# Optimization experiments

Hardware: AMD Instinct MI355X
Metric: run time of the kernel (lower is better)

The kernel has to match this reference:

```python
import jax, jax.numpy as jnp
import numpy as np

B, T, C = 2, 4096, 768
H = 12
D = C // H  # head_dim = 64

def setup_inputs() -> dict:
    key = jax.random.key(0)
    ks = jax.random.split(key, 5)
    s = 1.0 / np.sqrt(C)
    return {
        "x": jax.random.normal(ks[0], (B, T, C), dtype=jnp.float32),
        "qkv_w": jax.random.normal(ks[1], (C, 3 * C), dtype=jnp.float32) * s,
        "qkv_b": jax.random.normal(ks[2], (3 * C,), dtype=jnp.float32) * 0.02,
        "out_w": jax.random.normal(ks[3], (C, C), dtype=jnp.float32) * s,
        "out_b": jax.random.normal(ks[4], (C,), dtype=jnp.float32) * 0.02,
    }

def reference(x, qkv_w, qkv_b, out_w, out_b):
    b, t, c = x.shape
    qkv = x @ qkv_w + qkv_b                      # [B,T,3C]
    q, k, v = jnp.split(qkv, 3, axis=-1)
    # [B,T,C] -> [B,H,T,D]
    q = q.reshape(b, t, H, D).transpose(0, 2, 1, 3)
    k = k.reshape(b, t, H, D).transpose(0, 2, 1, 3)
    v = v.reshape(b, t, H, D).transpose(0, 2, 1, 3)
    scale = 1.0 / np.sqrt(D)
    attn = jnp.einsum('bhqd,bhkd->bhqk', q, k) * scale  # [B,H,T,T]
    causal = jnp.tril(jnp.ones((t, t), dtype=bool))
    attn = jnp.where(causal, attn, -jnp.inf)
    attn = jax.nn.softmax(attn, axis=-1)
    y = jnp.einsum('bhqk,bhkd->bhqd', attn, v)           # [B,H,T,D]
    y = y.transpose(0, 2, 1, 3).reshape(b, t, c)
    return y @ out_w + out_b
```

## Files before the change

### kernel.cpp

```cpp
#include <hip/hip_runtime.h>
#include <hip/hip_bf16.h>

#define T_SEQ 4096
#define C_DIM 768
#define H_NUM 12
#define D_HEAD 64
#define N3    2304
#define BHN   24

typedef __bf16 bf16x8 __attribute__((ext_vector_type(8)));
typedef float  f32x4  __attribute__((ext_vector_type(4)));
typedef unsigned int u32x4v __attribute__((ext_vector_type(4)));

__device__ inline unsigned short f2b(float f) {
    unsigned int x = __float_as_uint(f);
    unsigned int r = (x + 0x7FFFu + ((x >> 16) & 1u)) >> 16;
    return (unsigned short)r;
}

__device__ inline unsigned int pack_trunc(float lo, float hi) {
    return __builtin_amdgcn_perm(__float_as_uint(hi), __float_as_uint(lo), 0x07060302u);
}

__device__ inline void load_lds16(const unsigned short* g, unsigned short* l) {
    __builtin_amdgcn_global_load_lds(
        (const __attribute__((address_space(1))) unsigned int*)(g),
        (__attribute__((address_space(3))) unsigned int*)(l),
        16, 0, 0);
}

__device__ inline void transpose_tile(const float* __restrict__ in,
                                      unsigned short* __restrict__ out,
                                      unsigned short* Ts, int k0, int n0,
                                      int R, int Cc, int tid)
{
    #pragma unroll
    for (int it = 0; it < 4; ++it) {
        int idx = tid + it * 256;
        int r = idx >> 4, c4 = idx & 15;
        float4 v = *reinterpret_cast<const float4*>(&in[(size_t)(k0 + r) * Cc + n0 + c4 * 4]);
        Ts[(c4 * 4 + 0) * 72 + r] = f2b(v.x);
        Ts[(c4 * 4 + 1) * 72 + r] = f2b(v.y);
        Ts[(c4 * 4 + 2) * 72 + r] = f2b(v.z);
        Ts[(c4 * 4 + 3) * 72 + r] = f2b(v.w);
    }
    __syncthreads();
    #pragma unroll
    for (int it = 0; it < 2; ++it) {
        int idx = tid + it * 256;
        int row = idx >> 3, ch = idx & 7;
        *reinterpret_cast<uint4*>(&out[(size_t)(n0 + row) * R + k0 + ch * 8]) =
            *reinterpret_cast<const uint4*>(&Ts[row * 72 + ch * 8]);
    }
}

__global__ __launch_bounds__(256) void prep(
    const float* __restrict__ x, const float* __restrict__ qkv_w,
    const float* __restrict__ out_w,
    unsigned short* __restrict__ xb, unsigned short* __restrict__ wtq,
    unsigned short* __restrict__ wto)
{
    __shared__ unsigned short Ts[64 * 72];
    const int b = blockIdx.x, tid = threadIdx.x;
    if (b < 6144) {
        int idx = b * 256 + tid;
        float4 v = reinterpret_cast<const float4*>(x)[idx];
        ushort4 u;
        u.x = f2b(v.x); u.y = f2b(v.y); u.z = f2b(v.z); u.w = f2b(v.w);
        reinterpret_cast<ushort4*>(xb)[idx] = u;
    } else if (b < 6576) {
        int bb = b - 6144;
        transpose_tile(qkv_w, wtq, Ts, (bb % 12) * 64, (bb / 12) * 64, C_DIM, N3, tid);
    } else {
        int bb = b - 6576;
        transpose_tile(out_w, wto, Ts, (bb % 12) * 64, (bb / 12) * 64, C_DIM, C_DIM, tid);
    }
}

__global__ __launch_bounds__(256) void qkv_gemm(
    const unsigned short* __restrict__ xb, const unsigned short* __restrict__ wt,
    const float* __restrict__ bias,
    unsigned short* __restrict__ Q, unsigned short* __restrict__ K,
    unsigned short* __restrict__ Vt)
{
    __shared__ unsigned short SH[128 * 128];
    unsigned short* As = SH;
    unsigned short* Bs = SH + 128 * 64;
    const int tid  = threadIdx.x;
    const int m0   = blockIdx.x * 128;
    const int n0   = blockIdx.y * 128;
    const int lane = tid & 63;
    const int wv   = tid >> 6;
    const int wr   = wv >> 1, wc = wv & 1;
    const int quad = lane >> 4;
    const int lr   = lane & 15;
    const int srow = lane >> 3;
    const int dch  = (lane & 7) ^ srow;

    f32x4 acc[4][4] = {};

    for (int kk = 0; kk < C_DIM; kk += 64) {
        __syncthreads();
        #pragma unroll
        for (int i = 0; i < 4; ++i) {
            int inst = wv * 4 + i;
            int r = inst * 8 + srow;
            load_lds16(xb + (size_t)(m0 + r) * C_DIM + kk + dch * 8, As + inst * 512);
            load_lds16(wt + (size_t)(n0 + r) * C_DIM + kk + dch * 8, Bs + inst * 512);
        }
        __syncthreads();
        #pragma unroll
        for (int k2 = 0; k2 < 2; ++k2) {
            bf16x8 af[4], bf[4];
            #pragma unroll
            for (int mt = 0; mt < 4; ++mt)
                af[mt] = *reinterpret_cast<const bf16x8*>(
                    &As[(wr * 64 + mt * 16 + lr) * 64 + (((k2 * 4 + quad) ^ (lr & 7)) * 8)]);
            #pragma unroll
            for (int nt = 0; nt < 4; ++nt)
                bf[nt] = *reinterpret_cast<const bf16x8*>(
                    &Bs[(wc * 64 + nt * 16 + lr) * 64 + (((k2 * 4 + quad) ^ (lr & 7)) * 8)]);
            #pragma unroll
            for (int mt = 0; mt < 4; ++mt)
                #pragma unroll
                for (int nt = 0; nt < 4; ++nt)
                    acc[mt][nt] = __builtin_amdgcn_mfma_f32_16x16x32_bf16(af[mt], bf[nt], acc[mt][nt], 0, 0, 0);
        }
    }

    const int whichblk = n0 / C_DIM;
    if (whichblk == 2) {
        __syncthreads();
        #pragma unroll
        for (int nt = 0; nt < 4; ++nt) {
            int dp = wc * 64 + nt * 16 + lr;
            float bj = bias[n0 + dp];
            #pragma unroll
            for (int mt = 0; mt < 4; ++mt) {
                int t0 = wr * 64 + mt * 16 + quad * 4;
                ushort4 u;
                u.x = f2b(acc[mt][nt][0] + bj);
                u.y = f2b(acc[mt][nt][1] + bj);
                u.z = f2b(acc[mt][nt][2] + bj);
                u.w = f2b(acc[mt][nt][3] + bj);
                int cs = (t0 >> 2) ^ ((dp & 15) << 1);
                *reinterpret_cast<ushort4*>(&SH[dp * 128 + cs * 4]) = u;
            }
        }
        __syncthreads();
        const int bb = m0 >> 12;
        const int t_base = m0 & 4095;
        const int h_base = (n0 - 2 * C_DIM) >> 6;
        #pragma unroll
        for (int i = 0; i < 8; ++i) {
            int idx = i * 256 + tid;
            int row = idx >> 4, cc = idx & 15;
            int tile = cc >> 3, cp = cc & 7;
            int G0 = tile * 16 + ((cp >> 2) << 3) + (cp & 3);
            int swz = (row & 15) << 1;
            uint2 lo = *reinterpret_cast<const uint2*>(&SH[row * 128 + ((G0 ^ swz) * 4)]);
            uint2 hi = *reinterpret_cast<const uint2*>(&SH[row * 128 + (((G0 + 4) ^ swz) * 4)]);
            uint4 val = {lo.x, lo.y, hi.x, hi.y};
            int head = h_base + (row >> 6);
            int d = row & 63;
            *reinterpret_cast<uint4*>(
                &Vt[((size_t)(bb * H_NUM + head) * D_HEAD + d) * T_SEQ +
                    t_base + tile * 64 + cp * 8]) = val;
        }
    } else {
        const int head0 = ((n0 % C_DIM) + wc * 64) >> 6;
        #pragma unroll
        for (int nt = 0; nt < 4; ++nt) {
            int d = nt * 16 + lr;
            float bj = bias[n0 + wc * 64 + nt * 16 + lr];
            #pragma unroll
            for (int mt = 0; mt < 4; ++mt) {
                #pragma unroll
                for (int reg = 0; reg < 4; ++reg) {
                    int i = m0 + wr * 64 + mt * 16 + quad * 4 + reg;
                    int bb = i >> 12, t = i & 4095;
                    float val = acc[mt][nt][reg] + bj;
                    size_t base = (size_t)(bb * H_NUM + head0) * T_SEQ + t;
                    if (whichblk == 0)
                        Q[base * D_HEAD + d] = f2b(val * 0.18033688011f);
                    else
                        K[base * D_HEAD + d] = f2b(val);
                }
            }
        }
    }
}

__global__ __launch_bounds__(256, 3) void flash_attn(
    const unsigned short* __restrict__ Q, const unsigned short* __restrict__ K,
    const unsigned short* __restrict__ Vt, unsigned short* __restrict__ Y,
    float* __restrict__ pO, float* __restrict__ pl)
{
    __shared__ unsigned short Ks[2][64 * 64];
    __shared__ unsigned short Vs[2][64 * 64];
    const int tid  = threadIdx.x;
    const int lane = tid & 63;
    const int wv   = tid >> 6;
    const int quad = lane >> 4;
    const int lr   = lane & 15;
    const int srow = lane >> 3;
    const int dch  = (lane & 7) ^ srow;

    const int bid = blockIdx.x;
    const int ip  = bid / BHN;
    const int bh  = bid % BHN;

    const unsigned short* Qb = Q  + (size_t)bh * T_SEQ * D_HEAD;
    const unsigned short* Kb = K  + (size_t)bh * T_SEQ * D_HEAD;
    const unsigned short* Vb = Vt + (size_t)bh * D_HEAD * T_SEQ;

    int njob, jqt[2], jk0[2], jk1[2], jpart[2];
    if (ip < 16) {
        njob = 2;
        jqt[0] = ip;      jk0[0] = 0; jk1[0] = 2 * ip + 2;  jpart[0] = 0;
        jqt[1] = 31 - ip; jk0[1] = 0; jk1[1] = 31 - 2 * ip; jpart[1] = 1;
    } else {
        njob = 1;
        jqt[0] = ip; jk0[0] = 2 * ip - 31; jk1[0] = 2 * ip + 2; jpart[0] = 2;
    }

    bf16x8 ones;
    #pragma unroll
    for (int i = 0; i < 8; ++i) ones[i] = (__bf16)1.0f;
    const f32x4 zf = {};

    const int bb = bh / H_NUM, hh = bh % H_NUM;

    int buf = 0;
    {
        int kt = jk0[0];
        #pragma unroll
        for (int i = 0; i < 2; ++i) {
            int inst = wv * 2 + i;
            int r = inst * 8 + srow;
            load_lds16(Kb + (size_t)(kt * 64 + r) * D_HEAD + dch * 8, Ks[0] + inst * 512);
            load_lds16(Vb + (size_t)r * T_SEQ + kt * 64 + dch * 8, Vs[0] + inst * 512);
        }
    }

    for (int job = 0; job < njob; ++job) {
        const int qt = jqt[job];
        const int q0 = qt * 128;
        const int diag0 = 2 * qt;
        const int lastk = 2 * qt + 1;
        const int k0 = jk0[job], k1 = jk1[job];

        bf16x8 bQ[2][2];
        #pragma unroll
        for (int h = 0; h < 2; ++h)
            #pragma unroll
            for (int k2 = 0; k2 < 2; ++k2)
                bQ[h][k2] = *reinterpret_cast<const bf16x8*>(
                    &Qb[(size_t)(q0 + h * 64 + wv * 16 + lr) * D_HEAD + k2 * 32 + quad * 8]);

        f32x4 oacc[2][4] = {};
        f32x4 lacc[2] = {};

        for (int kt = k0; kt < k1; ++kt) {
            __syncthreads();

            int nkt = (kt + 1 < k1) ? (kt + 1) : ((job + 1 < njob) ? jk0[job + 1] : -1);
            if (nkt >= 0) {
                #pragma unroll
                for (int i = 0; i < 2; ++i) {
                    int inst = wv * 2 + i;
                    int r = inst * 8 + srow;
                    load_lds16(Kb + (size_t)(nkt * 64 + r) * D_HEAD + dch * 8,
                               Ks[buf ^ 1] + inst * 512);
                    load_lds16(Vb + (size_t)r * T_SEQ + nkt * 64 + dch * 8,
                               Vs[buf ^ 1] + inst * 512);
                }
            }

            const bool doh0 = (kt <= diag0);

            bf16x8 aK[4][2];
            #pragma unroll
            for (int mt = 0; mt < 4; ++mt)
                #pragma unroll
                for (int k2 = 0; k2 < 2; ++k2)
                    aK[mt][k2] = *reinterpret_cast<const bf16x8*>(
                        &Ks[buf][(mt * 16 + lr) * 64 + (((k2 * 4 + quad) ^ (lr & 7)) * 8)]);

            f32x4 st0[4], st1[4];
            #pragma unroll
            for (int mt = 0; mt < 4; ++mt) {
                st1[mt] = __builtin_amdgcn_mfma_f32_16x16x32_bf16(aK[mt][0], bQ[1][0], zf, 0, 0, 0);
                st1[mt] = __builtin_amdgcn_mfma_f32_16x16x32_bf16(aK[mt][1], bQ[1][1], st1[mt], 0, 0, 0);
            }
            if (doh0) {
                #pragma unroll
                for (int mt = 0; mt < 4; ++mt) {
                    st0[mt] = __builtin_amdgcn_mfma_f32_16x16x32_bf16(aK[mt][0], bQ[0][0], zf, 0, 0, 0);
                    st0[mt] = __builtin_amdgcn_mfma_f32_16x16x32_bf16(aK[mt][1], bQ[0][1], st0[mt], 0, 0, 0);
                }
            }

            bf16x8 aV[4][2];
            #pragma unroll
            for (int dt = 0; dt < 4; ++dt)
                #pragma unroll
                for (int f = 0; f < 2; ++f)
                    aV[dt][f] = *reinterpret_cast<const bf16x8*>(
                        &Vs[buf][(dt * 16 + lr) * 64 + (((f * 4 + quad) ^ (lr & 7)) * 8)]);

            if (kt == diag0) {
                int qg = q0 + wv * 16 + lr;
                #pragma unroll
                for (int mt = 0; mt < 4; ++mt)
                    #pragma unroll
                    for (int reg = 0; reg < 4; ++reg)
                        if (kt * 64 + mt * 16 + quad * 4 + reg > qg) st0[mt][reg] = -INFINITY;
            }
            if (kt == lastk) {
                int qg = q0 + 64 + wv * 16 + lr;
                #pragma unroll
                for (int mt = 0; mt < 4; ++mt)
                    #pragma unroll
                    for (int reg = 0; reg < 4; ++reg)
                        if (kt * 64 + mt * 16 + quad * 4 + reg > qg) st1[mt][reg] = -INFINITY;
            }

            bf16x8 bP1a, bP1b, bP0a, bP0b;
            {
                #pragma unroll
                for (int mt = 0; mt < 4; ++mt)
                    #pragma unroll
                    for (int reg = 0; reg < 4; ++reg)
                        st1[mt][reg] = __builtin_amdgcn_exp2f(st1[mt][reg]);
                u32x4v u;
                u[0] = pack_trunc(st1[0][0], st1[0][1]);
                u[1] = pack_trunc(st1[0][2], st1[0][3]);
                u[2] = pack_trunc(st1[1][0], st1[1][1]);
                u[3] = pack_trunc(st1[1][2], st1[1][3]);
                bP1a = __builtin_bit_cast(bf16x8, u);
                u[0] = pack_trunc(st1[2][0], st1[2][1]);
                u[1] = pack_trunc(st1[2][2], st1[2][3]);
                u[2] = pack_trunc(st1[3][0], st1[3][1]);
                u[3] = pack_trunc(st1[3][2], st1[3][3]);
                bP1b = __builtin_bit_cast(bf16x8, u);
            }
            if (doh0) {
                #pragma unroll
                for (int mt = 0; mt < 4; ++mt)
                    #pragma unroll
                    for (int reg = 0; reg < 4; ++reg)
                        st0[mt][reg] = __builtin_amdgcn_exp2f(st0[mt][reg]);
                u32x4v u;
                u[0] = pack_trunc(st0[0][0], st0[0][1]);
                u[1] = pack_trunc(st0[0][2], st0[0][3]);
                u[2] = pack_trunc(st0[1][0], st0[1][1]);
                u[3] = pack_trunc(st0[1][2], st0[1][3]);
                bP0a = __builtin_bit_cast(bf16x8, u);
                u[0] = pack_trunc(st0[2][0], st0[2][1]);
                u[1] = pack_trunc(st0[2][2], st0[2][3]);
                u[2] = pack_trunc(st0[3][0], st0[3][1]);
                u[3] = pack_trunc(st0[3][2], st0[3][3]);
                bP0b = __builtin_bit_cast(bf16x8, u);
            }

            if (doh0) {
                #pragma unroll
                for (int dt = 0; dt < 4; ++dt) {
                    oacc[0][dt] = __builtin_amdgcn_mfma_f32_16x16x32_bf16(aV[dt][0], bP0a, oacc[0][dt], 0, 0, 0);
                    oacc[0][dt] = __builtin_amdgcn_mfma_f32_16x16x32_bf16(aV[dt][1], bP0b, oacc[0][dt], 0, 0, 0);
                }
                lacc[0] = __builtin_amdgcn_mfma_f32_16x16x32_bf16(ones, bP0a, lacc[0], 0, 0, 0);
                lacc[0] = __builtin_amdgcn_mfma_f32_16x16x32_bf16(ones, bP0b, lacc[0], 0, 0, 0);
            }
            {
                #pragma unroll
                for (int dt = 0; dt < 4; ++dt) {
                    oacc[1][dt] = __builtin_amdgcn_mfma_f32_16x16x32_bf16(aV[dt][0], bP1a, oacc[1][dt], 0, 0, 0);
                    oacc[1][dt] = __builtin_amdgcn_mfma_f32_16x16x32_bf16(aV[dt][1], bP1b, oacc[1][dt], 0, 0, 0);
                }
                lacc[1] = __builtin_amdgcn_mfma_f32_16x16x32_bf16(ones, bP1a, lacc[1], 0, 0, 0);
                lacc[1] = __builtin_amdgcn_mfma_f32_16x16x32_bf16(ones, bP1b, lacc[1], 0, 0, 0);
            }

            buf ^= 1;
        }

        if (jpart[job] == 0) {
            #pragma unroll
            for (int h = 0; h < 2; ++h) {
                float inv = 1.f / lacc[h][0];
                int q = q0 + h * 64 + wv * 16 + lr;
                #pragma unroll
                for (int dt = 0; dt < 4; ++dt) {
                    ushort4 u;
                    u.x = f2b(oacc[h][dt][0] * inv);
                    u.y = f2b(oacc[h][dt][1] * inv);
                    u.z = f2b(oacc[h][dt][2] * inv);
                    u.w = f2b(oacc[h][dt][3] * inv);
                    *reinterpret_cast<ushort4*>(
                        &Y[(size_t)(bb * T_SEQ + q) * C_DIM + hh * 64 + dt * 16 + quad * 4]) = u;
                }
            }
        } else {
            const int slot = jpart[job] - 1;
            const int iH = 31 - qt;
            const size_t s = (size_t)slot * 384 + (size_t)bh * 16 + iH;
            float* po  = pO + s * 8192;
            float* plp = pl + s * 128;
            #pragma unroll
            for (int h = 0; h < 2; ++h) {
                int q = h * 64 + wv * 16 + lr;
                if (quad == 0) plp[q] = lacc[h][0];
                #pragma unroll
                for (int dt = 0; dt < 4; ++dt)
                    *reinterpret_cast<f32x4*>(&po[(size_t)q * 64 + dt * 16 + quad * 4]) = oacc[h][dt];
            }
        }
    }
}

__global__ __launch_bounds__(256) void combine(
    const float* __restrict__ pO, const float* __restrict__ pl,
    unsigned short* __restrict__ Y)
{
    const int s   = blockIdx.x;
    const int tid = threadIdx.x;
    const int bh  = s / 16, iH = s % 16;
    const int qt  = 31 - iH;
    const int bb  = bh / H_NUM, hh = bh % H_NUM;
    const int q0  = qt * 128;
    const float* a  = pO + (size_t)s * 8192;
    const float* b  = pO + (size_t)(384 + s) * 8192;
    const float* la = pl + (size_t)s * 128;
    const float* lb = pl + (size_t)(384 + s) * 128;
    #pragma unroll
    for (int j = 0; j < 8; ++j) {
        int idx = tid + j * 256;
        int f = idx * 4;
        int q = f >> 6, d0 = f & 63;
        float4 va = *reinterpret_cast<const float4*>(&a[f]);
        float4 vb = *reinterpret_cast<const float4*>(&b[f]);
        float inv = 1.f / (la[q] + lb[q]);
        ushort4 u;
        u.x = f2b((va.x + vb.x) * inv);
        u.y = f2b((va.y + vb.y) * inv);
        u.z = f2b((va.z + vb.z) * inv);
        u.w = f2b((va.w + vb.w) * inv);
        *reinterpret_cast<ushort4*>(
            &Y[(size_t)(bb * T_SEQ + q0 + q) * C_DIM + hh * 64 + d0]) = u;
    }
}

__global__ __launch_bounds__(256) void out_gemm(
    const unsigned short* __restrict__ Y, const unsigned short* __restrict__ wt,
    const float* __restrict__ bias, float* __restrict__ out)
{
    __shared__ unsigned short As[128 * 64];
    __shared__ unsigned short Bs[64 * 64];
    const int tid  = threadIdx.x;
    const int m0   = blockIdx.x * 128;
    const int n0   = blockIdx.y * 64;
    const int lane = tid & 63;
    const int wv   = tid >> 6;
    const int wr   = wv >> 1, wc = wv & 1;
    const int quad = lane >> 4;
    const int lr   = lane & 15;
    const int srow = lane >> 3;
    const int dch  = (lane & 7) ^ srow;

    f32x4 acc[4][2] = {};

    for (int kk = 0; kk < C_DIM; kk += 64) {
        __syncthreads();
        #pragma unroll
        for (int i = 0; i < 4; ++i) {
            int inst = wv * 4 + i;
            int r = inst * 8 + srow;
            load_lds16(Y + (size_t)(m0 + r) * C_DIM + kk + dch * 8, As + inst * 512);
        }
        #pragma unroll
        for (int i = 0; i < 2; ++i) {
            int inst = wv * 2 + i;
            int r = inst * 8 + srow;
            load_lds16(wt + (size_t)(n0 + r) * C_DIM + kk + dch * 8, Bs + inst * 512);
        }
        __syncthreads();
        #pragma unroll
        for (int k2 = 0; k2 < 2; ++k2) {
            bf16x8 af[4], bf[2];
            #pragma unroll
            for (int mt = 0; mt < 4; ++mt)
                af[mt] = *reinterpret_cast<const bf16x8*>(
                    &As[(wr * 64 + mt * 16 + lr) * 64 + (((k2 * 4 + quad) ^ (lr & 7)) * 8)]);
            #pragma unroll
            for (int nt = 0; nt < 2; ++nt)
                bf[nt] = *reinterpret_cast<const bf16x8*>(
                    &Bs[(wc * 32 + nt * 16 + lr) * 64 + (((k2 * 4 + quad) ^ (lr & 7)) * 8)]);
            #pragma unroll
            for (int mt = 0; mt < 4; ++mt)
                #pragma unroll
                for (int nt = 0; nt < 2; ++nt)
                    acc[mt][nt] = __builtin_amdgcn_mfma_f32_16x16x32_bf16(af[mt], bf[nt], acc[mt][nt], 0, 0, 0);
        }
    }

    #pragma unroll
    for (int nt = 0; nt < 2; ++nt) {
        int j = n0 + wc * 32 + nt * 16 + lr;
        float bj = bias[j];
        #pragma unroll
        for (int mt = 0; mt < 4; ++mt)
            #pragma unroll
            for (int reg = 0; reg < 4; ++reg) {
                int i = m0 + wr * 64 + mt * 16 + quad * 4 + reg;
                out[(size_t)i * C_DIM + j] = acc[mt][nt][reg] + bj;
            }
    }
}

extern "C" void kernel_launch(void* const* d_in, const int* in_sizes, int n_in,
                              void* d_out, int out_size, void* d_ws, size_t ws_size,
                              hipStream_t stream) {
    const float* x     = (const float*)d_in[0];
    const float* qkv_w = (const float*)d_in[1];
    const float* qkv_b = (const float*)d_in[2];
    const float* out_w = (const float*)d_in[3];
    const float* out_b = (const float*)d_in[4];
    float* out = (float*)d_out;

    unsigned short* xb  = (unsigned short*)d_ws;
    unsigned short* wtq = xb  + (size_t)8192 * 768;
    unsigned short* wto = wtq + (size_t)2304 * 768;
    unsigned short* Qs  = wto + (size_t)768 * 768;
    unsigned short* Kg  = Qs  + (size_t)BHN * T_SEQ * D_HEAD;
    unsigned short* Vt  = Kg  + (size_t)BHN * T_SEQ * D_HEAD;
    float*          pO  = (float*)(Vt + (size_t)BHN * T_SEQ * D_HEAD);
    float*          pl  = pO + (size_t)2 * 384 * 8192;
    unsigned short* Y   = xb;

    prep      <<<6720, 256, 0, stream>>>(x, qkv_w, out_w, xb, wtq, wto);
    qkv_gemm  <<<dim3(64, 18), 256, 0, stream>>>(xb, wtq, qkv_b, Qs, Kg, Vt);
    flash_attn<<<dim3(32 * BHN), 256, 0, stream>>>(Qs, Kg, Vt, Y, pO, pl);
    combine   <<<384, 256, 0, stream>>>(pO, pl, Y);
    out_gemm  <<<dim3(64, 12), 256, 0, stream>>>(Y, wto, out_b, out);
}
```

Measured before the change: 218.6 us.

## Split causal attention work into equal-size stream-K chunks across 1024 blocks

Replaces the paired q-tile scheduling with a stream-K style partition: the total causal KV-tile iterations are divided evenly over 1024 blocks, and each block decodes and walks across (head, q-tile) boundaries. Partial results are written as bf16 instead of fp32 and merged by a combine kernel that sums a variable number of chunks. Occupancy hint is raised to 4 blocks per CU. The aim is better load balance across CUs and less partial-buffer traffic, at the cost of more partial tiles, job-decode overhead, and reduced precision in the partial accumulators.

```diff
diff --git a/kernel.cpp b/kernel.cpp
--- a/kernel.cpp
+++ b/kernel.cpp
@@ -7,6 +7,8 @@
 #define D_HEAD 64
 #define N3    2304
 #define BHN   24
+#define NCHUNK 1024
+#define TOT_IT 25344
 
 typedef __bf16 bf16x8 __attribute__((ext_vector_type(8)));
 typedef float  f32x4  __attribute__((ext_vector_type(4)));
@@ -16,6 +18,10 @@
     unsigned int x = __float_as_uint(f);
     unsigned int r = (x + 0x7FFFu + ((x >> 16) & 1u)) >> 16;
     return (unsigned short)r;
+}
+
+__device__ inline float b2f(unsigned short u) {
+    return __uint_as_float(((unsigned int)u) << 16);
 }
 
 __device__ inline unsigned int pack_trunc(float lo, float hi) {
@@ -27,6 +33,21 @@
         (const __attribute__((address_space(1))) unsigned int*)(g),
         (__attribute__((address_space(3))) unsigned int*)(l),
         16, 0, 0);
+}
+
+__device__ inline void decode_job(int F, int Fe, int& bh, int& qt, int& kl0, int& kl1) {
+    bh = F / 1056;
+    int Floc = F - bh * 1056;
+    int qv = (int)((__builtin_sqrtf((float)(4 * Floc + 1)) - 1.0f) * 0.5f);
+    while ((qv + 1) * (qv + 2) <= Floc) ++qv;
+    while (qv * (qv + 1) > Floc) --qv;
+    qt = qv;
+    int T0 = qv * (qv + 1);
+    int sz = 2 * qv + 2;
+    kl0 = Floc - T0;
+    int lend = Fe - bh * 1056;
+    int tend = T0 + sz;
+    kl1 = (lend < tend ? lend : tend) - T0;
 }
 
 __device__ inline void transpose_tile(const float* __restrict__ in,
@@ -191,10 +212,10 @@
     }
 }
 
-__global__ __launch_bounds__(256, 3) void flash_attn(
+__global__ __launch_bounds__(256, 4) void flash_attn(
     const unsigned short* __restrict__ Q, const unsigned short* __restrict__ K,
     const unsigned short* __restrict__ Vt, unsigned short* __restrict__ Y,
-    float* __restrict__ pO, float* __restrict__ pl)
+    unsigned short* __restrict__ pO, float* __restrict__ pl)
 {
     __shared__ unsigned short Ks[2][64 * 64];
     __shared__ unsigned short Vs[2][64 * 64];
@@ -207,48 +228,42 @@
     const int dch  = (lane & 7) ^ srow;
 
     const int bid = blockIdx.x;
-    const int ip  = bid / BHN;
-    const int bh  = bid % BHN;
-
-    const unsigned short* Qb = Q  + (size_t)bh * T_SEQ * D_HEAD;
-    const unsigned short* Kb = K  + (size_t)bh * T_SEQ * D_HEAD;
-    const unsigned short* Vb = Vt + (size_t)bh * D_HEAD * T_SEQ;
-
-    int njob, jqt[2], jk0[2], jk1[2], jpart[2];
-    if (ip < 16) {
-        njob = 2;
-        jqt[0] = ip;      jk0[0] = 0; jk1[0] = 2 * ip + 2;  jpart[0] = 0;
-        jqt[1] = 31 - ip; jk0[1] = 0; jk1[1] = 31 - 2 * ip; jpart[1] = 1;
-    } else {
-        njob = 1;
-        jqt[0] = ip; jk0[0] = 2 * ip - 31; jk1[0] = 2 * ip + 2; jpart[0] = 2;
-    }
+    const int c   = ((bid & 7) << 7) | (bid >> 3);
+    int F  = (99 * c) >> 2;
+    const int Fe = (99 * (c + 1)) >> 2;
 
     bf16x8 ones;
     #pragma unroll
     for (int i = 0; i < 8; ++i) ones[i] = (__bf16)1.0f;
     const f32x4 zf = {};
 
-    const int bb = bh / H_NUM, hh = bh % H_NUM;
-
-    int buf = 0;
+    int bh, qt, kl0, kl1;
+    decode_job(F, Fe, bh, qt, kl0, kl1);
+
     {
-        int kt = jk0[0];
+        const unsigned short* Kb0 = K  + (size_t)bh * T_SEQ * D_HEAD;
+        const unsigned short* Vb0 = Vt + (size_t)bh * D_HEAD * T_SEQ;
         #pragma unroll
         for (int i = 0; i < 2; ++i) {
             int inst = wv * 2 + i;
             int r = inst * 8 + srow;
-            load_lds16(Kb + (size_t)(kt * 64 + r) * D_HEAD + dch * 8, Ks[0] + inst * 512);
-            load_lds16(Vb + (size_t)r * T_SEQ + kt * 64 + dch * 8, Vs[0] + inst * 512);
-        }
-    }
-
-    for (int job = 0; job < njob; ++job) {
-        const int qt = jqt[job];
+            load_lds16(Kb0 + (size_t)(kl0 * 64 + r) * D_HEAD + dch * 8, Ks[0] + inst * 512);
+            load_lds16(Vb0 + (size_t)r * T_SEQ + kl0 * 64 + dch * 8, Vs[0] + inst * 512);
+        }
+    }
+
+    int buf = 0;
+    while (true) {
+        int Fn = bh * 1056 + qt * (qt + 1) + kl1;
+        int nbh = -1, nqt = 0, nkl0 = 0, nkl1 = 0;
+        if (Fn < Fe) decode_job(Fn, Fe, nbh, nqt, nkl0, nkl1);
+
         const int q0 = qt * 128;
         const int diag0 = 2 * qt;
         const int lastk = 2 * qt + 1;
-        const int k0 = jk0[job], k1 = jk1[job];
+        const unsigned short* Qb = Q  + (size_t)bh * T_SEQ * D_HEAD;
+        const unsigned short* Kb = K  + (size_t)bh * T_SEQ * D_HEAD;
+        const unsigned short* Vb = Vt + (size_t)bh * D_HEAD * T_SEQ;
 
         bf16x8 bQ[2][2];
         #pragma unroll
@@ -261,18 +276,21 @@
         f32x4 oacc[2][4] = {};
         f32x4 lacc[2] = {};
 
-        for (int kt = k0; kt < k1; ++kt) {
+        for (int kt = kl0; kt < kl1; ++kt) {
             __syncthreads();
 
-            int nkt = (kt + 1 < k1) ? (kt + 1) : ((job + 1 < njob) ? jk0[job + 1] : -1);
-            if (nkt >= 0) {
+            int pbh = (kt + 1 < kl1) ? bh : nbh;
+            int pkt = (kt + 1 < kl1) ? (kt + 1) : nkl0;
+            if (pbh >= 0) {
+                const unsigned short* Kn = K  + (size_t)pbh * T_SEQ * D_HEAD;
+                const unsigned short* Vn = Vt + (size_t)pbh * D_HEAD * T_SEQ;
                 #pragma unroll
                 for (int i = 0; i < 2; ++i) {
                     int inst = wv * 2 + i;
                     int r = inst * 8 + srow;
-                    load_lds16(Kb + (size_t)(nkt * 64 + r) * D_HEAD + dch * 8,
+                    load_lds16(Kn + (size_t)(pkt * 64 + r) * D_HEAD + dch * 8,
                                Ks[buf ^ 1] + inst * 512);
-                    load_lds16(Vb + (size_t)r * T_SEQ + nkt * 64 + dch * 8,
+                    load_lds16(Vn + (size_t)r * T_SEQ + pkt * 64 + dch * 8,
                                Vs[buf ^ 1] + inst * 512);
                 }
             }
@@ -386,7 +404,9 @@
             buf ^= 1;
         }
 
-        if (jpart[job] == 0) {
+        const int bb = bh / H_NUM, hh = bh % H_NUM;
+        const int sz = 2 * qt + 2;
+        if (kl0 == 0 && kl1 == sz) {
             #pragma unroll
             for (int h = 0; h < 2; ++h) {
                 float inv = 1.f / lacc[h][0];
@@ -403,52 +423,71 @@
                 }
             }
         } else {
-            const int slot = jpart[job] - 1;
-            const int iH = 31 - qt;
-            const size_t s = (size_t)slot * 384 + (size_t)bh * 16 + iH;
-            float* po  = pO + s * 8192;
-            float* plp = pl + s * 128;
+            const int slot = (kl0 > 0) ? 0 : 1;
+            unsigned short* po = pO + ((size_t)c * 2 + slot) * 8192;
+            float* plp = pl + ((size_t)c * 2 + slot) * 128;
             #pragma unroll
             for (int h = 0; h < 2; ++h) {
                 int q = h * 64 + wv * 16 + lr;
                 if (quad == 0) plp[q] = lacc[h][0];
                 #pragma unroll
-                for (int dt = 0; dt < 4; ++dt)
-                    *reinterpret_cast<f32x4*>(&po[(size_t)q * 64 + dt * 16 + quad * 4]) = oacc[h][dt];
-            }
-        }
+                for (int dt = 0; dt < 4; ++dt) {
+                    ushort4 u;
+                    u.x = f2b(oacc[h][dt][0]);
+                    u.y = f2b(oacc[h][dt][1]);
+                    u.z = f2b(oacc[h][dt][2]);
+                    u.w = f2b(oacc[h][dt][3]);
+                    *reinterpret_cast<ushort4*>(&po[q * 64 + dt * 16 + quad * 4]) = u;
+                }
+            }
+        }
+
+        if (nbh < 0) break;
+        bh = nbh; qt = nqt; kl0 = nkl0; kl1 = nkl1;
     }
 }
 
 __global__ __launch_bounds__(256) void combine(
-    const float* __restrict__ pO, const float* __restrict__ pl,
+    const unsigned short* __restrict__ pO, const float* __restrict__ pl,
     unsigned short* __restrict__ Y)
 {
-    const int s   = blockIdx.x;
+    const int s  = blockIdx.x;
+    const int bh = s >> 5, qt = s & 31;
+    const int T0g = bh * 1056 + qt * (qt + 1);
+    const int T1g = T0g + 2 * qt + 2;
+    const int c0 = (4 * T0g + 3) / 99;
+    const int c1 = (4 * (T1g - 1) + 3) / 99;
+    if (c0 == c1) return;
+
     const int tid = threadIdx.x;
-    const int bh  = s / 16, iH = s % 16;
-    const int qt  = 31 - iH;
-    const int bb  = bh / H_NUM, hh = bh % H_NUM;
-    const int q0  = qt * 128;
-    const float* a  = pO + (size_t)s * 8192;
-    const float* b  = pO + (size_t)(384 + s) * 8192;
-    const float* la = pl + (size_t)s * 128;
-    const float* lb = pl + (size_t)(384 + s) * 128;
+    const int bb = bh / H_NUM, hh = bh % H_NUM;
+    const int q0 = qt * 128;
     #pragma unroll
     for (int j = 0; j < 8; ++j) {
         int idx = tid + j * 256;
-        int f = idx * 4;
-        int q = f >> 6, d0 = f & 63;
-        float4 va = *reinterpret_cast<const float4*>(&a[f]);
-        float4 vb = *reinterpret_cast<const float4*>(&b[f]);
-        float inv = 1.f / (la[q] + lb[q]);
-        ushort4 u;
-        u.x = f2b((va.x + vb.x) * inv);
-        u.y = f2b((va.y + vb.y) * inv);
-        u.z = f2b((va.z + vb.z) * inv);
-        u.w = f2b((va.w + vb.w) * inv);
+        int q = idx >> 4;
+        int d0 = (idx & 15) * 4;
+        float4 acc = {0.f, 0.f, 0.f, 0.f};
+        float lsum = 0.f;
+        for (int cc = c0; cc <= c1; ++cc) {
+            int sc = (99 * cc) >> 2;
+            int slot = (sc <= T0g) ? 1 : 0;
+            size_t base = (size_t)cc * 2 + slot;
+            ushort4 u = *reinterpret_cast<const ushort4*>(&pO[base * 8192 + (size_t)idx * 4]);
+            acc.x += b2f(u.x);
+            acc.y += b2f(u.y);
+            acc.z += b2f(u.z);
+            acc.w += b2f(u.w);
+            lsum += pl[base * 128 + q];
+        }
+        float inv = 1.f / lsum;
+        ushort4 o;
+        o.x = f2b(acc.x * inv);
+        o.y = f2b(acc.y * inv);
+        o.z = f2b(acc.z * inv);
+        o.w = f2b(acc.w * inv);
         *reinterpret_cast<ushort4*>(
-            &Y[(size_t)(bb * T_SEQ + q0 + q) * C_DIM + hh * 64 + d0]) = u;
+            &Y[(size_t)(bb * T_SEQ + q0 + q) * C_DIM + hh * 64 + d0]) = o;
     }
 }
 
@@ -535,13 +574,13 @@
     unsigned short* Qs  = wto + (size_t)768 * 768;
     unsigned short* Kg  = Qs  + (size_t)BHN * T_SEQ * D_HEAD;
     unsigned short* Vt  = Kg  + (size_t)BHN * T_SEQ * D_HEAD;
-    float*          pO  = (float*)(Vt + (size_t)BHN * T_SEQ * D_HEAD);
-    float*          pl  = pO + (size_t)2 * 384 * 8192;
+    unsigned short* pO  = Vt  + (size_t)BHN * T_SEQ * D_HEAD;
+    float*          pl  = (float*)(pO + (size_t)NCHUNK * 2 * 8192);
     unsigned short* Y   = xb;
 
     prep      <<<6720, 256, 0, stream>>>(x, qkv_w, out_w, xb, wtq, wto);
     qkv_gemm  <<<dim3(64, 18), 256, 0, stream>>>(xb, wtq, qkv_b, Qs, Kg, Vt);
-    flash_attn<<<dim3(32 * BHN), 256, 0, stream>>>(Qs, Kg, Vt, Y, pO, pl);
-    combine   <<<384, 256, 0, stream>>>(pO, pl, Y);
+    flash_attn<<<dim3(NCHUNK), 256, 0, stream>>>(Qs, Kg, Vt, Y, pO, pl);
+    combine   <<<768, 256, 0, stream>>>(pO, pl, Y);
     out_gemm  <<<dim3(64, 12), 256, 0, stream>>>(Y, wto, out_b, out);
 }
```

Measured after the change: 318.0 us. 1.45x slower.

## Store split-K attention partials in bf16 and raise wave priority around MFMA blocks

Applied to the files above, without the earlier changes.

The unnormalized partial outputs written by flash_attn for split query tiles are now stored as bf16 instead of fp32, and the combine kernel reads and widens them, halving the partial-output write and read traffic. The flash loop also wraps its two MFMA groups in s_setprio(1)/s_setprio(0) so waves issuing matrix ops get scheduling priority over waves doing softmax or loads. The bf16 partials lose some precision before normalization.

```diff
diff --git a/kernel.cpp b/kernel.cpp
--- a/kernel.cpp
+++ b/kernel.cpp
@@ -16,6 +16,10 @@
     unsigned int x = __float_as_uint(f);
     unsigned int r = (x + 0x7FFFu + ((x >> 16) & 1u)) >> 16;
     return (unsigned short)r;
+}
+
+__device__ inline float b2f(unsigned short u) {
+    return __uint_as_float(((unsigned int)u) << 16);
 }
 
 __device__ inline unsigned int pack_trunc(float lo, float hi) {
@@ -194,7 +198,7 @@
 __global__ __launch_bounds__(256, 3) void flash_attn(
     const unsigned short* __restrict__ Q, const unsigned short* __restrict__ K,
     const unsigned short* __restrict__ Vt, unsigned short* __restrict__ Y,
-    float* __restrict__ pO, float* __restrict__ pl)
+    unsigned short* __restrict__ pO, float* __restrict__ pl)
 {
     __shared__ unsigned short Ks[2][64 * 64];
     __shared__ unsigned short Vs[2][64 * 64];
@@ -288,6 +292,7 @@
                         &Ks[buf][(mt * 16 + lr) * 64 + (((k2 * 4 + quad) ^ (lr & 7)) * 8)]);
 
             f32x4 st0[4], st1[4];
+            __builtin_amdgcn_s_setprio(1);
             #pragma unroll
             for (int mt = 0; mt < 4; ++mt) {
                 st1[mt] = __builtin_amdgcn_mfma_f32_16x16x32_bf16(aK[mt][0], bQ[1][0], zf, 0, 0, 0);
@@ -300,6 +305,7 @@
                     st0[mt] = __builtin_amdgcn_mfma_f32_16x16x32_bf16(aK[mt][1], bQ[0][1], st0[mt], 0, 0, 0);
                 }
             }
+            __builtin_amdgcn_s_setprio(0);
 
             bf16x8 aV[4][2];
             #pragma unroll
@@ -364,6 +370,7 @@
                 bP0b = __builtin_bit_cast(bf16x8, u);
             }
 
+            __builtin_amdgcn_s_setprio(1);
             if (doh0) {
                 #pragma unroll
                 for (int dt = 0; dt < 4; ++dt) {
@@ -382,6 +389,7 @@
                 lacc[1] = __builtin_amdgcn_mfma_f32_16x16x32_bf16(ones, bP1a, lacc[1], 0, 0, 0);
                 lacc[1] = __builtin_amdgcn_mfma_f32_16x16x32_bf16(ones, bP1b, lacc[1], 0, 0, 0);
             }
+            __builtin_amdgcn_s_setprio(0);
 
             buf ^= 1;
         }
@@ -406,22 +414,28 @@
             const int slot = jpart[job] - 1;
             const int iH = 31 - qt;
             const size_t s = (size_t)slot * 384 + (size_t)bh * 16 + iH;
-            float* po  = pO + s * 8192;
+            unsigned short* po = pO + s * 8192;
             float* plp = pl + s * 128;
             #pragma unroll
             for (int h = 0; h < 2; ++h) {
                 int q = h * 64 + wv * 16 + lr;
                 if (quad == 0) plp[q] = lacc[h][0];
                 #pragma unroll
-                for (int dt = 0; dt < 4; ++dt)
-                    *reinterpret_cast<f32x4*>(&po[(size_t)q * 64 + dt * 16 + quad * 4]) = oacc[h][dt];
+                for (int dt = 0; dt < 4; ++dt) {
+                    ushort4 u;
+                    u.x = f2b(oacc[h][dt][0]);
+                    u.y = f2b(oacc[h][dt][1]);
+                    u.z = f2b(oacc[h][dt][2]);
+                    u.w = f2b(oacc[h][dt][3]);
+                    *reinterpret_cast<ushort4*>(&po[q * 64 + dt * 16 + quad * 4]) = u;
+                }
             }
         }
     }
 }
 
 __global__ __launch_bounds__(256) void combine(
-    const float* __restrict__ pO, const float* __restrict__ pl,
+    const unsigned short* __restrict__ pO, const float* __restrict__ pl,
     unsigned short* __restrict__ Y)
 {
     const int s   = blockIdx.x;
@@ -430,8 +444,8 @@
     const int qt  = 31 - iH;
     const int bb  = bh / H_NUM, hh = bh % H_NUM;
     const int q0  = qt * 128;
-    const float* a  = pO + (size_t)s * 8192;
-    const float* b  = pO + (size_t)(384 + s) * 8192;
+    const unsigned short* a = pO + (size_t)s * 8192;
+    const unsigned short* b = pO + (size_t)(384 + s) * 8192;
     const float* la = pl + (size_t)s * 128;
     const float* lb = pl + (size_t)(384 + s) * 128;
     #pragma unroll
@@ -439,14 +453,14 @@
         int idx = tid + j * 256;
         int f = idx * 4;
         int q = f >> 6, d0 = f & 63;
-        float4 va = *reinterpret_cast<const float4*>(&a[f]);
-        float4 vb = *reinterpret_cast<const float4*>(&b[f]);
+        ushort4 ua = *reinterpret_cast<const ushort4*>(&a[f]);
+        ushort4 ub = *reinterpret_cast<const ushort4*>(&b[f]);
         float inv = 1.f / (la[q] + lb[q]);
         ushort4 u;
-        u.x = f2b((va.x + vb.x) * inv);
-        u.y = f2b((va.y + vb.y) * inv);
-        u.z = f2b((va.z + vb.z) * inv);
-        u.w = f2b((va.w + vb.w) * inv);
+        u.x = f2b((b2f(ua.x) + b2f(ub.x)) * inv);
+        u.y = f2b((b2f(ua.y) + b2f(ub.y)) * inv);
+        u.z = f2b((b2f(ua.z) + b2f(ub.z)) * inv);
+        u.w = f2b((b2f(ua.w) + b2f(ub.w)) * inv);
         *reinterpret_cast<ushort4*>(
             &Y[(size_t)(bb * T_SEQ + q0 + q) * C_DIM + hh * 64 + d0]) = u;
     }
@@ -535,8 +549,8 @@
     unsigned short* Qs  = wto + (size_t)768 * 768;
     unsigned short* Kg  = Qs  + (size_t)BHN * T_SEQ * D_HEAD;
     unsigned short* Vt  = Kg  + (size_t)BHN * T_SEQ * D_HEAD;
-    float*          pO  = (float*)(Vt + (size_t)BHN * T_SEQ * D_HEAD);
-    float*          pl  = pO + (size_t)2 * 384 * 8192;
+    unsigned short* pO  = Vt  + (size_t)BHN * T_SEQ * D_HEAD;
+    float*          pl  = (float*)(pO + (size_t)2 * 384 * 8192);
     unsigned short* Y   = xb;
 
     prep      <<<6720, 256, 0, stream>>>(x, qkv_w, out_w, xb, wtq, wto);
```

Result: no change. 216.0 us (-1.2%).
